# Kernel optimization log

Hardware: AMD Instinct MI355X
Metric: run time of the kernel (lower is better)

## Reference

```python
import jax, jax.numpy as jnp
import numpy as np

EMBED_DIM = 256
NUM_HEADS = 8
HEAD_DIM = EMBED_DIM // NUM_HEADS
LN_EPS = 1e-5


def _linear_init(key, fan_in, fan_out):
    # torch nn.Linear default: U(-1/sqrt(fan_in), 1/sqrt(fan_in)) for W and b
    kw, kb = jax.random.split(key)
    bound = 1.0 / np.sqrt(fan_in)
    W = jax.random.uniform(kw, (fan_out, fan_in), jnp.float32, -bound, bound)
    b = jax.random.uniform(kb, (fan_out,), jnp.float32, -bound, bound)
    return W, b


def setup_inputs() -> dict:
    key = jax.random.key(0)
    ks = jax.random.split(key, 6)
    x = jax.random.normal(ks[0], (2, 512, EMBED_DIM), jnp.float32)
    Wq, bq = _linear_init(ks[1], EMBED_DIM, EMBED_DIM)
    Wk, bk = _linear_init(ks[2], EMBED_DIM, EMBED_DIM)
    Wv, bv = _linear_init(ks[3], EMBED_DIM, EMBED_DIM)
    Wr, br = _linear_init(ks[4], EMBED_DIM, EMBED_DIM)
    Wo, bo = _linear_init(ks[5], EMBED_DIM, EMBED_DIM)
    g1 = jnp.ones((EMBED_DIM,), jnp.float32)
    b1 = jnp.zeros((EMBED_DIM,), jnp.float32)
    g2 = jnp.ones((EMBED_DIM,), jnp.float32)
    b2 = jnp.zeros((EMBED_DIM,), jnp.float32)
    return {"x": x, "Wq": Wq, "bq": bq, "Wk": Wk, "bk": bk, "Wv": Wv, "bv": bv,
            "Wr": Wr, "br": br, "Wo": Wo, "bo": bo,
            "g1": g1, "b1": b1, "g2": g2, "b2": b2}


def _layer_norm(x, g, b):
    mu = jnp.mean(x, axis=-1, keepdims=True)
    var = jnp.mean(jnp.square(x - mu), axis=-1, keepdims=True)
    return (x - mu) * jax.lax.rsqrt(var + LN_EPS) * g + b


def reference(x, Wq, bq, Wk, bk, Wv, bv, Wr, br, Wo, bo, g1, b1, g2, b2):
    B, N, D = x.shape
    H, Dh = NUM_HEADS, HEAD_DIM
    Q = x @ Wq.T + bq  # [B,N,D]
    K = x @ Wk.T + bk
    V = x @ Wv.T + bv
    # pairwise differences, projected: [B,N,N,D]
    R = x[:, :, None, :] - x[:, None, :, :]
    R = jnp.einsum('bijd,ed->bije', R, Wr) + br
    max_R1 = jnp.max(R, axis=1)  # [B,N,D] (max over rows -> bias for Q)
    max_R2 = jnp.max(R, axis=2)  # [B,N,D] (max over cols -> bias for K)
    Q_r = Q + max_R1
    K_r = K + max_R2
    # [B,H,N,Dh]
    Q_r = Q_r.reshape(B, N, H, Dh).transpose(0, 2, 1, 3)
    K_r = K_r.reshape(B, N, H, Dh).transpose(0, 2, 1, 3)
    Vh = V.reshape(B, N, H, Dh).transpose(0, 2, 1, 3)
    scores = jnp.einsum('bhqd,bhkd->bhqk', Q_r, K_r) / np.sqrt(Dh).astype(np.float32)
    probs = jax.nn.softmax(scores, axis=-1)
    attn = jnp.einsum('bhqk,bhkd->bhqd', probs, Vh)
    attn = attn.transpose(0, 2, 1, 3).reshape(B, N, D)
    attn = attn @ Wo.T + bo  # dropout is identity in eval mode
    h = _layer_norm(x + attn, g1, b1)
    return _layer_norm(h, g2, b2)
```

## Files before the change

kernel.cpp:

```cpp
#include <hip/hip_runtime.h>
#include <hip/hip_bf16.h>
#include <math.h>

#define NSEQ 512
#define EMB 256

typedef __attribute__((ext_vector_type(8))) short bf16x8;
typedef __attribute__((ext_vector_type(4))) float f32x4;

__device__ __forceinline__ unsigned fenc(float f) {
    unsigned u = __float_as_uint(f);
    return (u & 0x80000000u) ? ~u : (u | 0x80000000u);
}
__device__ __forceinline__ float fdec(unsigned e) {
    unsigned u = (e & 0x80000000u) ? (e ^ 0x80000000u) : ~e;
    return __uint_as_float(u);
}

__device__ __forceinline__ unsigned short f2bf(float f) {
    unsigned u = __float_as_uint(f);
    unsigned r = (u + 0x7FFFu + ((u >> 16) & 1u)) >> 16;
    return (unsigned short)r;
}
__device__ __forceinline__ float bf2f(unsigned short s) {
    return __uint_as_float(((unsigned)s) << 16);
}

__global__ __launch_bounds__(256) void k_prep(
    const float* __restrict__ X,
    const float* __restrict__ Wq, const float* __restrict__ Wk,
    const float* __restrict__ Wv, const float* __restrict__ Wr,
    const float* __restrict__ Wo,
    unsigned short* __restrict__ Xb, unsigned short* __restrict__ Wallb,
    unsigned short* __restrict__ Wob, unsigned* __restrict__ maxEnc)
{
    const int t = threadIdx.x;
    const int idx4 = blockIdx.x * 256 + t;
    if (blockIdx.x == 0) { maxEnc[t] = 0u; maxEnc[256 + t] = 0u; }
    if (idx4 >= 147456) return;

    float4 v;
    ushort4* dst;
    if (idx4 < 65536) {
        v = ((const float4*)X)[idx4];
        dst = &((ushort4*)Xb)[idx4];
    } else if (idx4 < 131072) {
        int j = idx4 - 65536;
        int row = j >> 6, c4 = j & 63;
        int seg = row >> 8, wr = row & 255;
        size_t off = (size_t)wr * 64 + c4;
        if (seg == 0) {
            float4 a = ((const float4*)Wq)[off], r = ((const float4*)Wr)[off];
            v = make_float4(a.x - r.x, a.y - r.y, a.z - r.z, a.w - r.w);
        } else if (seg == 1) {
            float4 a = ((const float4*)Wk)[off], r = ((const float4*)Wr)[off];
            v = make_float4(a.x + r.x, a.y + r.y, a.z + r.z, a.w + r.w);
        } else if (seg == 2) {
            v = ((const float4*)Wv)[off];
        } else {
            v = ((const float4*)Wr)[off];
        }
        dst = &((ushort4*)Wallb)[j];
    } else {
        int j = idx4 - 131072;
        v = ((const float4*)Wo)[j];
        dst = &((ushort4*)Wob)[j];
    }
    ushort4 o;
    o.x = f2bf(v.x); o.y = f2bf(v.y); o.z = f2bf(v.z); o.w = f2bf(v.w);
    *dst = o;
}

__global__ __launch_bounds__(256) void k_gemm_mfma(
    const unsigned short* __restrict__ Xb,
    const unsigned short* __restrict__ Wallb,
    const float* __restrict__ bq, const float* __restrict__ bv,
    unsigned short* __restrict__ Qb, unsigned short* __restrict__ Kb,
    unsigned short* __restrict__ Vtb, unsigned* __restrict__ maxEnc)
{
    __shared__ __align__(16) unsigned short Xs[64 * 264];
    __shared__ __align__(16) unsigned short Ws[64 * 264];
    __shared__ float red[4][64];

    const int t = threadIdx.x;
    const int w = t >> 6, l = t & 63;
    const int ln = l & 15, kg = l >> 4;
    const int m0 = blockIdx.x * 64;
    const int nW = blockIdx.y * 64;
    const int seg = blockIdx.y >> 2;

    const uint4* Xg = (const uint4*)Xb;
    const uint4* Wg = (const uint4*)Wallb;
    #pragma unroll
    for (int i = 0; i < 8; ++i) {
        int idx = i * 256 + t;
        int row = idx >> 5, c8 = idx & 31;
        *(uint4*)(Xs + row * 264 + c8 * 8) = Xg[(size_t)(m0 + row) * 32 + c8];
        *(uint4*)(Ws + row * 264 + c8 * 8) = Wg[(size_t)(nW + row) * 32 + c8];
    }
    __syncthreads();

    f32x4 acc[4] = {{0.f,0.f,0.f,0.f},{0.f,0.f,0.f,0.f},
                    {0.f,0.f,0.f,0.f},{0.f,0.f,0.f,0.f}};
    const int arow = (w << 4) + ln;
    #pragma unroll
    for (int ks = 0; ks < 8; ++ks) {
        bf16x8 a = *(const bf16x8*)(Xs + arow * 264 + ks * 32 + kg * 8);
        #pragma unroll
        for (int nf = 0; nf < 4; ++nf) {
            bf16x8 b = *(const bf16x8*)(Ws + (nf * 16 + ln) * 264 + ks * 32 + kg * 8);
            acc[nf] = __builtin_amdgcn_mfma_f32_16x16x32_bf16(a, b, acc[nf], 0, 0, 0);
        }
    }

    if (seg == 0) {
        #pragma unroll
        for (int nf = 0; nf < 4; ++nf) {
            int c = (nW & 255) + nf * 16 + ln;
            float bb = bq[c];
            #pragma unroll
            for (int r = 0; r < 4; ++r) {
                int row = m0 + w * 16 + kg * 4 + r;
                Qb[(size_t)row * 256 + c] = f2bf(acc[nf][r] + bb);
            }
        }
    } else if (seg == 1) {
        #pragma unroll
        for (int nf = 0; nf < 4; ++nf) {
            int c = (nW & 255) + nf * 16 + ln;
            #pragma unroll
            for (int r = 0; r < 4; ++r) {
                int row = m0 + w * 16 + kg * 4 + r;
                Kb[(size_t)row * 256 + c] = f2bf(acc[nf][r]);
            }
        }
    } else if (seg == 2) {
        #pragma unroll
        for (int nf = 0; nf < 4; ++nf) {
            int c = (nW & 255) + nf * 16 + ln;
            int h = c >> 5, d = c & 31;
            float bb = bv[c];
            #pragma unroll
            for (int r = 0; r < 4; ++r) {
                int row = m0 + w * 16 + kg * 4 + r;
                int b = row >> 9, ml = row & 511;
                Vtb[((size_t)(b * 8 + h) * 32 + d) * 512 + ml] = f2bf(acc[nf][r] + bb);
            }
        }
    } else {
        #pragma unroll
        for (int nf = 0; nf < 4; ++nf) {
            float mx = fmaxf(fmaxf(acc[nf][0], acc[nf][1]),
                             fmaxf(acc[nf][2], acc[nf][3]));
            mx = fmaxf(mx, __shfl_xor(mx, 16));
            mx = fmaxf(mx, __shfl_xor(mx, 32));
            if (l < 16) red[w][nf * 16 + ln] = mx;
        }
        __syncthreads();
        if (t < 64) {
            float m = fmaxf(fmaxf(red[0][t], red[1][t]),
                            fmaxf(red[2][t], red[3][t]));
            atomicMax(&maxEnc[(m0 >> 9) * 256 + (nW & 255) + t], fenc(m));
        }
    }
}

__global__ __launch_bounds__(256) void k_attn_mfma(
    const unsigned short* __restrict__ Qb,
    const unsigned short* __restrict__ Kb,
    const unsigned short* __restrict__ Vtb,
    const unsigned* __restrict__ maxEnc,
    const float* __restrict__ br,
    unsigned short* __restrict__ attnb)
{
    __shared__ __align__(16) unsigned short Plds[4][16][136];
    __shared__ float Olds[4][16][33];
    __shared__ float mlds[4][16], llds[4][16];
    __shared__ float scl[4][16], Li[16];

    const int t = threadIdx.x;
    const int w = t >> 6, l = t & 63;
    const int ln = l & 15, kg = l >> 4;
    const int q0 = blockIdx.x * 16;
    const int h = blockIdx.y, b = blockIdx.z;
    const int e0 = h * 32;
    const int bh = b * 8 + h;
    const float scale = 0.17677669529663687f;

    bf16x8 af;
    {
        size_t qrow = (size_t)(b * NSEQ + q0 + ln) * 256 + e0 + kg * 8;
        bf16x8 qa = *(const bf16x8*)(Qb + qrow);
        #pragma unroll
        for (int j = 0; j < 8; ++j) {
            int d = kg * 8 + j;
            float qv = bf2f((unsigned short)qa[j]);
            float ad = fdec(maxEnc[b * 256 + e0 + d]) + br[e0 + d];
            af[j] = (short)f2bf((qv + ad) * scale);
        }
    }

    const int key0 = w * 128;
    f32x4 sc[8];
    #pragma unroll
    for (int kf = 0; kf < 8; ++kf) {
        size_t krow = (size_t)(b * NSEQ + key0 + kf * 16 + ln) * 256 + e0 + kg * 8;
        bf16x8 bfr = *(const bf16x8*)(Kb + krow);
        f32x4 z = {0.f, 0.f, 0.f, 0.f};
        sc[kf] = __builtin_amdgcn_mfma_f32_16x16x32_bf16(af, bfr, z, 0, 0, 0);
    }

    float m_[4], l_[4];
    #pragma unroll
    for (int r = 0; r < 4; ++r) {
        float mx = sc[0][r];
        #pragma unroll
        for (int kf = 1; kf < 8; ++kf) mx = fmaxf(mx, sc[kf][r]);
        #pragma unroll
        for (int off = 1; off < 16; off <<= 1) mx = fmaxf(mx, __shfl_xor(mx, off));
        m_[r] = mx;
        float s = 0.f;
        #pragma unroll
        for (int kf = 0; kf < 8; ++kf) {
            float p = __expf(sc[kf][r] - mx);
            sc[kf][r] = p;
            s += p;
        }
        #pragma unroll
        for (int off = 1; off < 16; off <<= 1) s += __shfl_xor(s, off);
        l_[r] = s;
    }

    #pragma unroll
    for (int kf = 0; kf < 8; ++kf)
        #pragma unroll
        for (int r = 0; r < 4; ++r)
            Plds[w][kg * 4 + r][kf * 16 + ln] = f2bf(sc[kf][r]);

    f32x4 o[2] = {{0.f,0.f,0.f,0.f},{0.f,0.f,0.f,0.f}};
    #pragma unroll
    for (int ks = 0; ks < 4; ++ks) {
        bf16x8 pf = *(const bf16x8*)&Plds[w][ln][ks * 32 + kg * 8];
        #pragma unroll
        for (int df = 0; df < 2; ++df) {
            size_t vrow = ((size_t)bh * 32 + df * 16 + ln) * 512 + key0 + ks * 32 + kg * 8;
            bf16x8 vf = *(const bf16x8*)(Vtb + vrow);
            o[df] = __builtin_amdgcn_mfma_f32_16x16x32_bf16(pf, vf, o[df], 0, 0, 0);
        }
    }

    if (ln == 0) {
        #pragma unroll
        for (int r = 0; r < 4; ++r) {
            mlds[w][kg * 4 + r] = m_[r];
            llds[w][kg * 4 + r] = l_[r];
        }
    }
    #pragma unroll
    for (int df = 0; df < 2; ++df)
        #pragma unroll
        for (int r = 0; r < 4; ++r)
            Olds[w][kg * 4 + r][df * 16 + ln] = o[df][r];
    __syncthreads();

    if (t < 16) {
        float M = fmaxf(fmaxf(mlds[0][t], mlds[1][t]),
                        fmaxf(mlds[2][t], mlds[3][t]));
        float L = 0.f;
        #pragma unroll
        for (int wv = 0; wv < 4; ++wv) {
            float s = __expf(mlds[wv][t] - M);
            scl[wv][t] = s;
            L += s * llds[wv][t];
        }
        Li[t] = 1.f / L;
    }
    __syncthreads();

    #pragma unroll
    for (int i = 0; i < 2; ++i) {
        int idx = t + 256 * i;
        int q = idx >> 5, d = idx & 31;
        float acc = 0.f;
        #pragma unroll
        for (int wv = 0; wv < 4; ++wv)
            acc += scl[wv][q] * Olds[wv][q][d];
        attnb[(size_t)(b * NSEQ + q0 + q) * 256 + e0 + d] = f2bf(acc * Li[q]);
    }
}

__global__ __launch_bounds__(256) void k_ogemm_mfma(
    const unsigned short* __restrict__ Ab,
    const unsigned short* __restrict__ Wob,
    float* __restrict__ yPart)
{
    __shared__ __align__(16) unsigned short As_[64 * 72];
    __shared__ __align__(16) unsigned short Bs_[64 * 72];

    const int t = threadIdx.x;
    const int w = t >> 6, l = t & 63;
    const int ln = l & 15, kg = l >> 4;
    const int m0 = blockIdx.x * 64;
    const int n0 = blockIdx.y * 64;
    const int bz = blockIdx.z;

    const uint4* Ag = (const uint4*)Ab;
    const uint4* Wg = (const uint4*)Wob;
    #pragma unroll
    for (int i = 0; i < 2; ++i) {
        int idx = i * 256 + t;
        int row = idx >> 3, c8 = idx & 7;
        *(uint4*)(As_ + row * 72 + c8 * 8) = Ag[(size_t)(m0 + row) * 32 + bz * 8 + c8];
        *(uint4*)(Bs_ + row * 72 + c8 * 8) = Wg[(size_t)(n0 + row) * 32 + bz * 8 + c8];
    }
    __syncthreads();

    f32x4 acc[4] = {{0.f,0.f,0.f,0.f},{0.f,0.f,0.f,0.f},
                    {0.f,0.f,0.f,0.f},{0.f,0.f,0.f,0.f}};
    const int arow = (w << 4) + ln;
    #pragma unroll
    for (int ks = 0; ks < 2; ++ks) {
        bf16x8 a = *(const bf16x8*)(As_ + arow * 72 + ks * 32 + kg * 8);
        #pragma unroll
        for (int nf = 0; nf < 4; ++nf) {
            bf16x8 b = *(const bf16x8*)(Bs_ + (nf * 16 + ln) * 72 + ks * 32 + kg * 8);
            acc[nf] = __builtin_amdgcn_mfma_f32_16x16x32_bf16(a, b, acc[nf], 0, 0, 0);
        }
    }

    float* dst = yPart + (size_t)bz * (1024 * 256);
    #pragma unroll
    for (int nf = 0; nf < 4; ++nf) {
        #pragma unroll
        for (int r = 0; r < 4; ++r) {
            int row = m0 + w * 16 + kg * 4 + r;
            dst[(size_t)row * 256 + n0 + nf * 16 + ln] = acc[nf][r];
        }
    }
}

__global__ __launch_bounds__(256) void k_lnorm(
    const float* __restrict__ yP, const float* __restrict__ x,
    const float* __restrict__ bo,
    const float* __restrict__ g1, const float* __restrict__ b1,
    const float* __restrict__ g2, const float* __restrict__ b2,
    float* __restrict__ out)
{
    __shared__ float red[4][4][2];
    const int t = threadIdx.x;
    const int r0 = blockIdx.x * 4;
    const int c = t;
    const int wid = t >> 6, lane = t & 63;

    float y[4];
    #pragma unroll
    for (int r = 0; r < 4; ++r) {
        size_t off = (size_t)(r0 + r) * 256 + c;
        y[r] = x[off] + bo[c] + yP[off] + yP[262144 + off]
             + yP[524288 + off] + yP[786432 + off];
    }

    #pragma unroll
    for (int r = 0; r < 4; ++r) {
        float s = y[r], s2 = y[r] * y[r];
        #pragma unroll
        for (int off = 32; off > 0; off >>= 1) {
            s  += __shfl_xor(s, off);
            s2 += __shfl_xor(s2, off);
        }
        if (lane == 0) { red[wid][r][0] = s; red[wid][r][1] = s2; }
    }
    __syncthreads();
    float t1[4];
    #pragma unroll
    for (int r = 0; r < 4; ++r) {
        float s  = red[0][r][0] + red[1][r][0] + red[2][r][0] + red[3][r][0];
        float s2 = red[0][r][1] + red[1][r][1] + red[2][r][1] + red[3][r][1];
        float mu = s * (1.f / 256.f);
        float var = s2 * (1.f / 256.f) - mu * mu;
        float rs = rsqrtf(var + 1e-5f);
        t1[r] = (y[r] - mu) * rs * g1[c] + b1[c];
    }
    __syncthreads();

    #pragma unroll
    for (int r = 0; r < 4; ++r) {
        float s = t1[r], s2 = t1[r] * t1[r];
        #pragma unroll
        for (int off = 32; off > 0; off >>= 1) {
            s  += __shfl_xor(s, off);
            s2 += __shfl_xor(s2, off);
        }
        if (lane == 0) { red[wid][r][0] = s; red[wid][r][1] = s2; }
    }
    __syncthreads();
    #pragma unroll
    for (int r = 0; r < 4; ++r) {
        float s  = red[0][r][0] + red[1][r][0] + red[2][r][0] + red[3][r][0];
        float s2 = red[0][r][1] + red[1][r][1] + red[2][r][1] + red[3][r][1];
        float mu = s * (1.f / 256.f);
        float var = s2 * (1.f / 256.f) - mu * mu;
        float rs = rsqrtf(var + 1e-5f);
        out[(size_t)(r0 + r) * 256 + c] = (t1[r] - mu) * rs * g2[c] + b2[c];
    }
}

extern "C" void kernel_launch(void* const* d_in, const int* in_sizes, int n_in,
                              void* d_out, int out_size, void* d_ws, size_t ws_size,
                              hipStream_t stream)
{
    const float* x  = (const float*)d_in[0];
    const float* Wq = (const float*)d_in[1];
    const float* bq = (const float*)d_in[2];
    const float* Wk = (const float*)d_in[3];
    const float* bk = (const float*)d_in[4];
    const float* Wv = (const float*)d_in[5];
    const float* bv = (const float*)d_in[6];
    const float* Wr = (const float*)d_in[7];
    const float* br = (const float*)d_in[8];
    const float* Wo = (const float*)d_in[9];
    const float* bo = (const float*)d_in[10];
    const float* g1 = (const float*)d_in[11];
    const float* b1 = (const float*)d_in[12];
    const float* g2 = (const float*)d_in[13];
    const float* b2 = (const float*)d_in[14];
    float* out = (float*)d_out;
    float* ws = (float*)d_ws;
    (void)bk;

    float* yP = ws;
    unsigned short* Xb    = (unsigned short*)(ws + 1048576);
    unsigned short* Wallb = (unsigned short*)(ws + 1179648);
    unsigned short* Wob   = (unsigned short*)(ws + 1310720);
    unsigned short* Qb    = (unsigned short*)(ws + 1343488);
    unsigned short* Kb    = (unsigned short*)(ws + 1474560);
    unsigned short* Vtb   = (unsigned short*)(ws + 1605632);
    unsigned short* attnb = (unsigned short*)(ws + 1736704);
    unsigned* maxEnc      = (unsigned*)(ws + 1867776);

    k_prep<<<576, 256, 0, stream>>>(x, Wq, Wk, Wv, Wr, Wo, Xb, Wallb, Wob, maxEnc);
    k_gemm_mfma<<<dim3(16, 16), 256, 0, stream>>>(Xb, Wallb, bq, bv,
                                                  Qb, Kb, Vtb, maxEnc);
    k_attn_mfma<<<dim3(32, 8, 2), 256, 0, stream>>>(Qb, Kb, Vtb, maxEnc, br, attnb);
    k_ogemm_mfma<<<dim3(16, 4, 4), 256, 0, stream>>>(attnb, Wob, yP);
    k_lnorm<<<256, 256, 0, stream>>>(yP, x, bo, g1, b1, g2, b2, out);
}
```

Before: 31.92 us.

## Fuse bf16 conversion into QKV GEMM and output GEMM with layer norms

```diff
diff --git a/kernel.cpp b/kernel.cpp
--- a/kernel.cpp
+++ b/kernel.cpp
@@ -25,78 +25,72 @@
 __device__ __forceinline__ float bf2f(unsigned short s) {
     return __uint_as_float(((unsigned)s) << 16);
 }
-
-__global__ __launch_bounds__(256) void k_prep(
+__device__ __forceinline__ ushort4 cvt4(float4 v) {
+    ushort4 o;
+    o.x = f2bf(v.x); o.y = f2bf(v.y); o.z = f2bf(v.z); o.w = f2bf(v.w);
+    return o;
+}
+
+__global__ __launch_bounds__(256) void k_gemm_mfma(
     const float* __restrict__ X,
     const float* __restrict__ Wq, const float* __restrict__ Wk,
     const float* __restrict__ Wv, const float* __restrict__ Wr,
     const float* __restrict__ Wo,
-    unsigned short* __restrict__ Xb, unsigned short* __restrict__ Wallb,
-    unsigned short* __restrict__ Wob, unsigned* __restrict__ maxEnc)
+    const float* __restrict__ bq, const float* __restrict__ bv,
+    unsigned short* __restrict__ Qb, unsigned short* __restrict__ Kb,
+    unsigned short* __restrict__ Vtb, unsigned short* __restrict__ Wob,
+    unsigned* __restrict__ maxEnc)
 {
     const int t = threadIdx.x;
-    const int idx4 = blockIdx.x * 256 + t;
-    if (blockIdx.x == 0) { maxEnc[t] = 0u; maxEnc[256 + t] = 0u; }
-    if (idx4 >= 147456) return;
-
-    float4 v;
-    ushort4* dst;
-    if (idx4 < 65536) {
-        v = ((const float4*)X)[idx4];
-        dst = &((ushort4*)Xb)[idx4];
-    } else if (idx4 < 131072) {
-        int j = idx4 - 65536;
-        int row = j >> 6, c4 = j & 63;
-        int seg = row >> 8, wr = row & 255;
-        size_t off = (size_t)wr * 64 + c4;
-        if (seg == 0) {
-            float4 a = ((const float4*)Wq)[off], r = ((const float4*)Wr)[off];
-            v = make_float4(a.x - r.x, a.y - r.y, a.z - r.z, a.w - r.w);
-        } else if (seg == 1) {
-            float4 a = ((const float4*)Wk)[off], r = ((const float4*)Wr)[off];
-            v = make_float4(a.x + r.x, a.y + r.y, a.z + r.z, a.w + r.w);
-        } else if (seg == 2) {
-            v = ((const float4*)Wv)[off];
-        } else {
-            v = ((const float4*)Wr)[off];
-        }
-        dst = &((ushort4*)Wallb)[j];
-    } else {
-        int j = idx4 - 131072;
-        v = ((const float4*)Wo)[j];
-        dst = &((ushort4*)Wob)[j];
-    }
-    ushort4 o;
-    o.x = f2bf(v.x); o.y = f2bf(v.y); o.z = f2bf(v.z); o.w = f2bf(v.w);
-    *dst = o;
-}
-
-__global__ __launch_bounds__(256) void k_gemm_mfma(
-    const unsigned short* __restrict__ Xb,
-    const unsigned short* __restrict__ Wallb,
-    const float* __restrict__ bq, const float* __restrict__ bv,
-    unsigned short* __restrict__ Qb, unsigned short* __restrict__ Kb,
-    unsigned short* __restrict__ Vtb, unsigned* __restrict__ maxEnc)
-{
+
+    if (blockIdx.y == 16) {
+        const float4* Wg = (const float4*)Wo;
+        #pragma unroll
+        for (int i = 0; i < 4; ++i) {
+            int idx4 = blockIdx.x * 1024 + i * 256 + t;
+            ((ushort4*)Wob)[idx4] = cvt4(Wg[idx4]);
+        }
+        return;
+    }
+
     __shared__ __align__(16) unsigned short Xs[64 * 264];
     __shared__ __align__(16) unsigned short Ws[64 * 264];
     __shared__ float red[4][64];
 
-    const int t = threadIdx.x;
     const int w = t >> 6, l = t & 63;
     const int ln = l & 15, kg = l >> 4;
     const int m0 = blockIdx.x * 64;
     const int nW = blockIdx.y * 64;
     const int seg = blockIdx.y >> 2;
-
-    const uint4* Xg = (const uint4*)Xb;
-    const uint4* Wg = (const uint4*)Wallb;
-    #pragma unroll
-    for (int i = 0; i < 8; ++i) {
+    const int wbase = (blockIdx.y & 3) * 64;
+
+    const float4* X4  = (const float4*)X;
+    const float4* Wq4 = (const float4*)Wq;
+    const float4* Wk4 = (const float4*)Wk;
+    const float4* Wv4 = (const float4*)Wv;
+    const float4* Wr4 = (const float4*)Wr;
+
+    #pragma unroll
+    for (int i = 0; i < 16; ++i) {
         int idx = i * 256 + t;
-        int row = idx >> 5, c8 = idx & 31;
-        *(uint4*)(Xs + row * 264 + c8 * 8) = Xg[(size_t)(m0 + row) * 32 + c8];
-        *(uint4*)(Ws + row * 264 + c8 * 8) = Wg[(size_t)(nW + row) * 32 + c8];
+        int row = idx >> 6, c4 = idx & 63;
+        float4 xv = X4[(size_t)(m0 + row) * 64 + c4];
+        *(ushort4*)(Xs + row * 264 + c4 * 4) = cvt4(xv);
+
+        size_t off = (size_t)(wbase + row) * 64 + c4;
+        float4 wv;
+        if (seg == 0) {
+            float4 a = Wq4[off], r = Wr4[off];
+            wv = make_float4(a.x - r.x, a.y - r.y, a.z - r.z, a.w - r.w);
+        } else if (seg == 1) {
+            float4 a = Wk4[off], r = Wr4[off];
+            wv = make_float4(a.x + r.x, a.y + r.y, a.z + r.z, a.w + r.w);
+        } else if (seg == 2) {
+            wv = Wv4[off];
+        } else {
+            wv = Wr4[off];
+        }
+        *(ushort4*)(Ws + row * 264 + c4 * 4) = cvt4(wv);
     }
     __syncthreads();
 
@@ -289,119 +283,94 @@
     }
 }
 
-__global__ __launch_bounds__(256) void k_ogemm_mfma(
+__global__ __launch_bounds__(256) void k_oln(
     const unsigned short* __restrict__ Ab,
     const unsigned short* __restrict__ Wob,
-    float* __restrict__ yPart)
-{
-    __shared__ __align__(16) unsigned short As_[64 * 72];
-    __shared__ __align__(16) unsigned short Bs_[64 * 72];
-
-    const int t = threadIdx.x;
-    const int w = t >> 6, l = t & 63;
-    const int ln = l & 15, kg = l >> 4;
-    const int m0 = blockIdx.x * 64;
-    const int n0 = blockIdx.y * 64;
-    const int bz = blockIdx.z;
-
-    const uint4* Ag = (const uint4*)Ab;
-    const uint4* Wg = (const uint4*)Wob;
-    #pragma unroll
-    for (int i = 0; i < 2; ++i) {
-        int idx = i * 256 + t;
-        int row = idx >> 3, c8 = idx & 7;
-        *(uint4*)(As_ + row * 72 + c8 * 8) = Ag[(size_t)(m0 + row) * 32 + bz * 8 + c8];
-        *(uint4*)(Bs_ + row * 72 + c8 * 8) = Wg[(size_t)(n0 + row) * 32 + bz * 8 + c8];
-    }
-    __syncthreads();
-
-    f32x4 acc[4] = {{0.f,0.f,0.f,0.f},{0.f,0.f,0.f,0.f},
-                    {0.f,0.f,0.f,0.f},{0.f,0.f,0.f,0.f}};
-    const int arow = (w << 4) + ln;
-    #pragma unroll
-    for (int ks = 0; ks < 2; ++ks) {
-        bf16x8 a = *(const bf16x8*)(As_ + arow * 72 + ks * 32 + kg * 8);
-        #pragma unroll
-        for (int nf = 0; nf < 4; ++nf) {
-            bf16x8 b = *(const bf16x8*)(Bs_ + (nf * 16 + ln) * 72 + ks * 32 + kg * 8);
-            acc[nf] = __builtin_amdgcn_mfma_f32_16x16x32_bf16(a, b, acc[nf], 0, 0, 0);
-        }
-    }
-
-    float* dst = yPart + (size_t)bz * (1024 * 256);
-    #pragma unroll
-    for (int nf = 0; nf < 4; ++nf) {
-        #pragma unroll
-        for (int r = 0; r < 4; ++r) {
-            int row = m0 + w * 16 + kg * 4 + r;
-            dst[(size_t)row * 256 + n0 + nf * 16 + ln] = acc[nf][r];
-        }
-    }
-}
-
-__global__ __launch_bounds__(256) void k_lnorm(
-    const float* __restrict__ yP, const float* __restrict__ x,
-    const float* __restrict__ bo,
+    const float* __restrict__ x, const float* __restrict__ bo,
     const float* __restrict__ g1, const float* __restrict__ b1,
     const float* __restrict__ g2, const float* __restrict__ b2,
     float* __restrict__ out)
 {
-    __shared__ float red[4][4][2];
+    __shared__ __align__(16) unsigned short As_[16 * 264];
+    __shared__ float ylds[16][257];
+
     const int t = threadIdx.x;
-    const int r0 = blockIdx.x * 4;
-    const int c = t;
-    const int wid = t >> 6, lane = t & 63;
-
-    float y[4];
-    #pragma unroll
-    for (int r = 0; r < 4; ++r) {
-        size_t off = (size_t)(r0 + r) * 256 + c;
-        y[r] = x[off] + bo[c] + yP[off] + yP[262144 + off]
-             + yP[524288 + off] + yP[786432 + off];
-    }
-
-    #pragma unroll
-    for (int r = 0; r < 4; ++r) {
-        float s = y[r], s2 = y[r] * y[r];
-        #pragma unroll
-        for (int off = 32; off > 0; off >>= 1) {
-            s  += __shfl_xor(s, off);
-            s2 += __shfl_xor(s2, off);
-        }
-        if (lane == 0) { red[wid][r][0] = s; red[wid][r][1] = s2; }
+    const int w = t >> 6, l = t & 63;
+    const int ln = l & 15, kg = l >> 4;
+    const int m0 = blockIdx.x * 16;
+
+    const uint4* Ag = (const uint4*)Ab;
+    #pragma unroll
+    for (int i = 0; i < 2; ++i) {
+        int idx = i * 256 + t;
+        int row = idx >> 5, c8 = idx & 31;
+        *(uint4*)(As_ + row * 264 + c8 * 8) = Ag[(size_t)(m0 + row) * 32 + c8];
     }
     __syncthreads();
-    float t1[4];
-    #pragma unroll
-    for (int r = 0; r < 4; ++r) {
-        float s  = red[0][r][0] + red[1][r][0] + red[2][r][0] + red[3][r][0];
-        float s2 = red[0][r][1] + red[1][r][1] + red[2][r][1] + red[3][r][1];
-        float mu = s * (1.f / 256.f);
-        float var = s2 * (1.f / 256.f) - mu * mu;
-        float rs = rsqrtf(var + 1e-5f);
-        t1[r] = (y[r] - mu) * rs * g1[c] + b1[c];
-    }
+
+    f32x4 acc[4] = {{0.f,0.f,0.f,0.f},{0.f,0.f,0.f,0.f},
+                    {0.f,0.f,0.f,0.f},{0.f,0.f,0.f,0.f}};
+    #pragma unroll
+    for (int ks = 0; ks < 8; ++ks) {
+        bf16x8 a = *(const bf16x8*)(As_ + ln * 264 + ks * 32 + kg * 8);
+        #pragma unroll
+        for (int nf = 0; nf < 4; ++nf) {
+            int n = w * 64 + nf * 16 + ln;
+            bf16x8 b = *(const bf16x8*)(Wob + (size_t)n * 256 + ks * 32 + kg * 8);
+            acc[nf] = __builtin_amdgcn_mfma_f32_16x16x32_bf16(a, b, acc[nf], 0, 0, 0);
+        }
+    }
+
+    #pragma unroll
+    for (int nf = 0; nf < 4; ++nf)
+        #pragma unroll
+        for (int r = 0; r < 4; ++r)
+            ylds[kg * 4 + r][w * 64 + nf * 16 + ln] = acc[nf][r];
     __syncthreads();
 
-    #pragma unroll
-    for (int r = 0; r < 4; ++r) {
-        float s = t1[r], s2 = t1[r] * t1[r];
-        #pragma unroll
-        for (int off = 32; off > 0; off >>= 1) {
-            s  += __shfl_xor(s, off);
-            s2 += __shfl_xor(s2, off);
-        }
-        if (lane == 0) { red[wid][r][0] = s; red[wid][r][1] = s2; }
-    }
-    __syncthreads();
-    #pragma unroll
-    for (int r = 0; r < 4; ++r) {
-        float s  = red[0][r][0] + red[1][r][0] + red[2][r][0] + red[3][r][0];
-        float s2 = red[0][r][1] + red[1][r][1] + red[2][r][1] + red[3][r][1];
-        float mu = s * (1.f / 256.f);
-        float var = s2 * (1.f / 256.f) - mu * mu;
-        float rs = rsqrtf(var + 1e-5f);
-        out[(size_t)(r0 + r) * 256 + c] = (t1[r] - mu) * rs * g2[c] + b2[c];
+    const int row = t >> 4, lc = t & 15;
+    const size_t gro = (size_t)(m0 + row) * 256;
+
+    float y[16];
+    float s = 0.f, s2 = 0.f;
+    #pragma unroll
+    for (int j = 0; j < 16; ++j) {
+        int c = lc + 16 * j;
+        float v = x[gro + c] + bo[c] + ylds[row][c];
+        y[j] = v;
+        s += v; s2 += v * v;
+    }
+    #pragma unroll
+    for (int off = 1; off < 16; off <<= 1) {
+        s  += __shfl_xor(s, off);
+        s2 += __shfl_xor(s2, off);
+    }
+    float mu = s * (1.f / 256.f);
+    float var = s2 * (1.f / 256.f) - mu * mu;
+    float rs = rsqrtf(var + 1e-5f);
+
+    float t1[16];
+    s = 0.f; s2 = 0.f;
+    #pragma unroll
+    for (int j = 0; j < 16; ++j) {
+        int c = lc + 16 * j;
+        float v = (y[j] - mu) * rs * g1[c] + b1[c];
+        t1[j] = v;
+        s += v; s2 += v * v;
+    }
+    #pragma unroll
+    for (int off = 1; off < 16; off <<= 1) {
+        s  += __shfl_xor(s, off);
+        s2 += __shfl_xor(s2, off);
+    }
+    mu = s * (1.f / 256.f);
+    var = s2 * (1.f / 256.f) - mu * mu;
+    rs = rsqrtf(var + 1e-5f);
+
+    #pragma unroll
+    for (int j = 0; j < 16; ++j) {
+        int c = lc + 16 * j;
+        out[gro + c] = (t1[j] - mu) * rs * g2[c] + b2[c];
     }
 }
 
@@ -425,23 +394,19 @@
     const float* g2 = (const float*)d_in[13];
     const float* b2 = (const float*)d_in[14];
     float* out = (float*)d_out;
-    float* ws = (float*)d_ws;
     (void)bk;
 
-    float* yP = ws;
-    unsigned short* Xb    = (unsigned short*)(ws + 1048576);
-    unsigned short* Wallb = (unsigned short*)(ws + 1179648);
-    unsigned short* Wob   = (unsigned short*)(ws + 1310720);
-    unsigned short* Qb    = (unsigned short*)(ws + 1343488);
-    unsigned short* Kb    = (unsigned short*)(ws + 1474560);
-    unsigned short* Vtb   = (unsigned short*)(ws + 1605632);
-    unsigned short* attnb = (unsigned short*)(ws + 1736704);
-    unsigned* maxEnc      = (unsigned*)(ws + 1867776);
-
-    k_prep<<<576, 256, 0, stream>>>(x, Wq, Wk, Wv, Wr, Wo, Xb, Wallb, Wob, maxEnc);
-    k_gemm_mfma<<<dim3(16, 16), 256, 0, stream>>>(Xb, Wallb, bq, bv,
-                                                  Qb, Kb, Vtb, maxEnc);
+    unsigned short* u = (unsigned short*)d_ws;
+    unsigned short* Qb    = u;
+    unsigned short* Kb    = u + 262144;
+    unsigned short* Vtb   = u + 524288;
+    unsigned short* attnb = u + 786432;
+    unsigned short* Wob   = u + 1048576;
+    unsigned* maxEnc = (unsigned*)(u + 1114112);
+
+    hipMemsetAsync(maxEnc, 0x00, 512 * sizeof(unsigned), stream);
+    k_gemm_mfma<<<dim3(16, 17), 256, 0, stream>>>(x, Wq, Wk, Wv, Wr, Wo, bq, bv,
+                                                  Qb, Kb, Vtb, Wob, maxEnc);
     k_attn_mfma<<<dim3(32, 8, 2), 256, 0, stream>>>(Qb, Kb, Vtb, maxEnc, br, attnb);
-    k_ogemm_mfma<<<dim3(16, 4, 4), 256, 0, stream>>>(attnb, Wob, yP);
-    k_lnorm<<<256, 256, 0, stream>>>(yP, x, bo, g1, b1, g2, b2, out);
-}
+    k_oln<<<64, 256, 0, stream>>>(attnb, Wob, x, bo, g1, b1, g2, b2, out);
+}
```

Measured after the change: 39.43 us. 1.24x slower.

## Fuse bf16 conversion into QKV GEMM and replace atomic max with partial-max buffer

Applied to the files above, without the earlier changes.

```diff
diff --git a/kernel.cpp b/kernel.cpp
--- a/kernel.cpp
+++ b/kernel.cpp
@@ -7,15 +7,6 @@
 
 typedef __attribute__((ext_vector_type(8))) short bf16x8;
 typedef __attribute__((ext_vector_type(4))) float f32x4;
-
-__device__ __forceinline__ unsigned fenc(float f) {
-    unsigned u = __float_as_uint(f);
-    return (u & 0x80000000u) ? ~u : (u | 0x80000000u);
-}
-__device__ __forceinline__ float fdec(unsigned e) {
-    unsigned u = (e & 0x80000000u) ? (e ^ 0x80000000u) : ~e;
-    return __uint_as_float(u);
-}
 
 __device__ __forceinline__ unsigned short f2bf(float f) {
     unsigned u = __float_as_uint(f);
@@ -25,78 +16,72 @@
 __device__ __forceinline__ float bf2f(unsigned short s) {
     return __uint_as_float(((unsigned)s) << 16);
 }
-
-__global__ __launch_bounds__(256) void k_prep(
+__device__ __forceinline__ ushort4 cvt4(float4 v) {
+    ushort4 o;
+    o.x = f2bf(v.x); o.y = f2bf(v.y); o.z = f2bf(v.z); o.w = f2bf(v.w);
+    return o;
+}
+
+__global__ __launch_bounds__(256) void k_gemm_mfma(
     const float* __restrict__ X,
     const float* __restrict__ Wq, const float* __restrict__ Wk,
     const float* __restrict__ Wv, const float* __restrict__ Wr,
     const float* __restrict__ Wo,
-    unsigned short* __restrict__ Xb, unsigned short* __restrict__ Wallb,
-    unsigned short* __restrict__ Wob, unsigned* __restrict__ maxEnc)
+    const float* __restrict__ bq, const float* __restrict__ bv,
+    unsigned short* __restrict__ Qb, unsigned short* __restrict__ Kb,
+    unsigned short* __restrict__ Vtb, unsigned short* __restrict__ Wob,
+    float* __restrict__ maxPart)
 {
     const int t = threadIdx.x;
-    const int idx4 = blockIdx.x * 256 + t;
-    if (blockIdx.x == 0) { maxEnc[t] = 0u; maxEnc[256 + t] = 0u; }
-    if (idx4 >= 147456) return;
-
-    float4 v;
-    ushort4* dst;
-    if (idx4 < 65536) {
-        v = ((const float4*)X)[idx4];
-        dst = &((ushort4*)Xb)[idx4];
-    } else if (idx4 < 131072) {
-        int j = idx4 - 65536;
-        int row = j >> 6, c4 = j & 63;
-        int seg = row >> 8, wr = row & 255;
-        size_t off = (size_t)wr * 64 + c4;
-        if (seg == 0) {
-            float4 a = ((const float4*)Wq)[off], r = ((const float4*)Wr)[off];
-            v = make_float4(a.x - r.x, a.y - r.y, a.z - r.z, a.w - r.w);
-        } else if (seg == 1) {
-            float4 a = ((const float4*)Wk)[off], r = ((const float4*)Wr)[off];
-            v = make_float4(a.x + r.x, a.y + r.y, a.z + r.z, a.w + r.w);
-        } else if (seg == 2) {
-            v = ((const float4*)Wv)[off];
-        } else {
-            v = ((const float4*)Wr)[off];
-        }
-        dst = &((ushort4*)Wallb)[j];
-    } else {
-        int j = idx4 - 131072;
-        v = ((const float4*)Wo)[j];
-        dst = &((ushort4*)Wob)[j];
-    }
-    ushort4 o;
-    o.x = f2bf(v.x); o.y = f2bf(v.y); o.z = f2bf(v.z); o.w = f2bf(v.w);
-    *dst = o;
-}
-
-__global__ __launch_bounds__(256) void k_gemm_mfma(
-    const unsigned short* __restrict__ Xb,
-    const unsigned short* __restrict__ Wallb,
-    const float* __restrict__ bq, const float* __restrict__ bv,
-    unsigned short* __restrict__ Qb, unsigned short* __restrict__ Kb,
-    unsigned short* __restrict__ Vtb, unsigned* __restrict__ maxEnc)
-{
+
+    if (blockIdx.y == 16) {
+        const float4* Wg = (const float4*)Wo;
+        #pragma unroll
+        for (int i = 0; i < 4; ++i) {
+            int idx4 = blockIdx.x * 1024 + i * 256 + t;
+            ((ushort4*)Wob)[idx4] = cvt4(Wg[idx4]);
+        }
+        return;
+    }
+
     __shared__ __align__(16) unsigned short Xs[64 * 264];
     __shared__ __align__(16) unsigned short Ws[64 * 264];
     __shared__ float red[4][64];
 
-    const int t = threadIdx.x;
     const int w = t >> 6, l = t & 63;
     const int ln = l & 15, kg = l >> 4;
     const int m0 = blockIdx.x * 64;
     const int nW = blockIdx.y * 64;
     const int seg = blockIdx.y >> 2;
-
-    const uint4* Xg = (const uint4*)Xb;
-    const uint4* Wg = (const uint4*)Wallb;
-    #pragma unroll
-    for (int i = 0; i < 8; ++i) {
+    const int wbase = (blockIdx.y & 3) * 64;
+
+    const float4* X4  = (const float4*)X;
+    const float4* Wq4 = (const float4*)Wq;
+    const float4* Wk4 = (const float4*)Wk;
+    const float4* Wv4 = (const float4*)Wv;
+    const float4* Wr4 = (const float4*)Wr;
+
+    #pragma unroll
+    for (int i = 0; i < 16; ++i) {
         int idx = i * 256 + t;
-        int row = idx >> 5, c8 = idx & 31;
-        *(uint4*)(Xs + row * 264 + c8 * 8) = Xg[(size_t)(m0 + row) * 32 + c8];
-        *(uint4*)(Ws + row * 264 + c8 * 8) = Wg[(size_t)(nW + row) * 32 + c8];
+        int row = idx >> 6, c4 = idx & 63;
+        float4 xv = X4[(size_t)(m0 + row) * 64 + c4];
+        *(ushort4*)(Xs + row * 264 + c4 * 4) = cvt4(xv);
+
+        size_t off = (size_t)(wbase + row) * 64 + c4;
+        float4 wv;
+        if (seg == 0) {
+            float4 a = Wq4[off], r = Wr4[off];
+            wv = make_float4(a.x - r.x, a.y - r.y, a.z - r.z, a.w - r.w);
+        } else if (seg == 1) {
+            float4 a = Wk4[off], r = Wr4[off];
+            wv = make_float4(a.x + r.x, a.y + r.y, a.z + r.z, a.w + r.w);
+        } else if (seg == 2) {
+            wv = Wv4[off];
+        } else {
+            wv = Wr4[off];
+        }
+        *(ushort4*)(Ws + row * 264 + c4 * 4) = cvt4(wv);
     }
     __syncthreads();
 
@@ -160,7 +145,9 @@
         if (t < 64) {
             float m = fmaxf(fmaxf(red[0][t], red[1][t]),
                             fmaxf(red[2][t], red[3][t]));
-            atomicMax(&maxEnc[(m0 >> 9) * 256 + (nW & 255) + t], fenc(m));
+            const int b = blockIdx.x >> 3;
+            const int mblk = blockIdx.x & 7;
+            maxPart[b * 2048 + mblk * 256 + (nW & 255) + t] = m;
         }
     }
 }
@@ -169,7 +156,7 @@
     const unsigned short* __restrict__ Qb,
     const unsigned short* __restrict__ Kb,
     const unsigned short* __restrict__ Vtb,
-    const unsigned* __restrict__ maxEnc,
+    const float* __restrict__ maxPart,
     const float* __restrict__ br,
     unsigned short* __restrict__ attnb)
 {
@@ -177,6 +164,7 @@
     __shared__ float Olds[4][16][33];
     __shared__ float mlds[4][16], llds[4][16];
     __shared__ float scl[4][16], Li[16];
+    __shared__ float qadd[32];
 
     const int t = threadIdx.x;
     const int w = t >> 6, l = t & 63;
@@ -187,6 +175,15 @@
     const int bh = b * 8 + h;
     const float scale = 0.17677669529663687f;
 
+    if (t < 32) {
+        float m = maxPart[b * 2048 + e0 + t];
+        #pragma unroll
+        for (int j = 1; j < 8; ++j)
+            m = fmaxf(m, maxPart[b * 2048 + j * 256 + e0 + t]);
+        qadd[t] = m + br[e0 + t];
+    }
+    __syncthreads();
+
     bf16x8 af;
     {
         size_t qrow = (size_t)(b * NSEQ + q0 + ln) * 256 + e0 + kg * 8;
@@ -195,8 +192,7 @@
         for (int j = 0; j < 8; ++j) {
             int d = kg * 8 + j;
             float qv = bf2f((unsigned short)qa[j]);
-            float ad = fdec(maxEnc[b * 256 + e0 + d]) + br[e0 + d];
-            af[j] = (short)f2bf((qv + ad) * scale);
+            af[j] = (short)f2bf((qv + qadd[d]) * scale);
         }
     }
 
@@ -425,23 +421,20 @@
     const float* g2 = (const float*)d_in[13];
     const float* b2 = (const float*)d_in[14];
     float* out = (float*)d_out;
-    float* ws = (float*)d_ws;
     (void)bk;
 
-    float* yP = ws;
-    unsigned short* Xb    = (unsigned short*)(ws + 1048576);
-    unsigned short* Wallb = (unsigned short*)(ws + 1179648);
-    unsigned short* Wob   = (unsigned short*)(ws + 1310720);
-    unsigned short* Qb    = (unsigned short*)(ws + 1343488);
-    unsigned short* Kb    = (unsigned short*)(ws + 1474560);
-    unsigned short* Vtb   = (unsigned short*)(ws + 1605632);
-    unsigned short* attnb = (unsigned short*)(ws + 1736704);
-    unsigned* maxEnc      = (unsigned*)(ws + 1867776);
-
-    k_prep<<<576, 256, 0, stream>>>(x, Wq, Wk, Wv, Wr, Wo, Xb, Wallb, Wob, maxEnc);
-    k_gemm_mfma<<<dim3(16, 16), 256, 0, stream>>>(Xb, Wallb, bq, bv,
-                                                  Qb, Kb, Vtb, maxEnc);
-    k_attn_mfma<<<dim3(32, 8, 2), 256, 0, stream>>>(Qb, Kb, Vtb, maxEnc, br, attnb);
+    unsigned short* u = (unsigned short*)d_ws;
+    unsigned short* Qb    = u;
+    unsigned short* Kb    = u + 262144;
+    unsigned short* Vtb   = u + 524288;
+    unsigned short* attnb = u + 786432;
+    unsigned short* Wob   = u + 1048576;
+    float* maxPart = (float*)(u + 1114112);
+    float* yP      = (float*)(u + 1122304);
+
+    k_gemm_mfma<<<dim3(16, 17), 256, 0, stream>>>(x, Wq, Wk, Wv, Wr, Wo, bq, bv,
+                                                  Qb, Kb, Vtb, Wob, maxPart);
+    k_attn_mfma<<<dim3(32, 8, 2), 256, 0, stream>>>(Qb, Kb, Vtb, maxPart, br, attnb);
     k_ogemm_mfma<<<dim3(16, 4, 4), 256, 0, stream>>>(attnb, Wob, yP);
     k_lnorm<<<256, 256, 0, stream>>>(yP, x, bo, g1, b1, g2, b2, out);
 }
```

Result: faster. 28.34 us (-11.2%).
